# Optimization experiments

Measured on AMD Instinct MI355X. Metric: run time of the kernel, lower is better.

Reference implementation:

```python
import jax, jax.numpy as jnp
import numpy as np
from math import sqrt

# Complete K-ary tree: level l has K**l nodes; children of node j at level l
# are nodes j*K .. j*K+K-1 of level l+1. Levels are processed leaves->root.
K = 4
LEVELS = 9
N_NODES = (K ** LEVELS - 1) // (K - 1)  # 87381
X_SIZE = 256
H_SIZE = 256
A_SIZE = 256
N_HEADS = 8
A_K = A_SIZE // N_HEADS


def setup_inputs() -> dict:
    key = jax.random.key(0)
    ks = jax.random.split(key, 20)
    s = 0.02
    d = {
        'x': jax.random.normal(ks[0], (N_NODES, X_SIZE), dtype=jnp.float32),
        'W_iou': jax.random.normal(ks[1], (X_SIZE, 3 * H_SIZE), dtype=jnp.float32) * s,
        'b_iou': jnp.zeros((3 * H_SIZE,), dtype=jnp.float32),
        'W_f': jax.random.normal(ks[2], (X_SIZE, H_SIZE), dtype=jnp.float32) * s,
        'b_f': jnp.zeros((H_SIZE,), dtype=jnp.float32),
        'Wq': jax.random.normal(ks[3], (X_SIZE, A_SIZE), dtype=jnp.float32) * s,
        'bq': jax.random.normal(ks[4], (A_SIZE,), dtype=jnp.float32) * s,
        'Wk': jax.random.normal(ks[5], (H_SIZE, A_SIZE), dtype=jnp.float32) * s,
        'bk': jax.random.normal(ks[6], (A_SIZE,), dtype=jnp.float32) * s,
        'Wv': jax.random.normal(ks[7], (H_SIZE, A_SIZE), dtype=jnp.float32) * s,
        'bv': jax.random.normal(ks[8], (A_SIZE,), dtype=jnp.float32) * s,
        'Wl': jax.random.normal(ks[9], (A_SIZE, A_SIZE), dtype=jnp.float32) * s,
        'bl': jax.random.normal(ks[10], (A_SIZE,), dtype=jnp.float32) * s,
        'Uiou_w': jax.random.normal(ks[11], (A_SIZE, 3 * H_SIZE), dtype=jnp.float32) * s,
        'Uiou_b': jax.random.normal(ks[12], (3 * H_SIZE,), dtype=jnp.float32) * s,
        'Uf_w': jax.random.normal(ks[13], (A_SIZE, H_SIZE), dtype=jnp.float32) * s,
        'Uf_b': jax.random.normal(ks[14], (H_SIZE,), dtype=jnp.float32) * s,
    }
    return d


def _tree_lstm(x, W_iou, b_iou, W_f, b_f, Wq, bq, Wk, bk, Wv, bv, Wl, bl,
               Uiou_w, Uiou_b, Uf_w, Uf_b):
    scale = 1.0 / sqrt(A_K)
    x_iou = x @ W_iou + b_iou          # [N, 3H]
    x_f = x @ W_f + b_f                # [N, H]
    starts = [(K ** l - 1) // (K - 1) for l in range(LEVELS)]
    h_lvl = [None] * LEVELS
    c_lvl = [None] * LEVELS
    for l in reversed(range(LEVELS)):
        s0 = starts[l]
        n = K ** l
        xi = x_iou[s0:s0 + n]
        xf = x_f[s0:s0 + n]
        if l == LEVELS - 1:  # leaves: empty mailbox
            iou = xi
            fc_sum = jnp.zeros((n, H_SIZE), dtype=x.dtype)
        else:
            ch_h = h_lvl[l + 1].reshape(n, K, H_SIZE)  # children mailbox 'h'
            ch_c = c_lvl[l + 1].reshape(n, K, H_SIZE)  # children mailbox 'c'
            q = (x[s0:s0 + n] @ Wq + bq).reshape(n, N_HEADS, A_K)
            kk = (ch_h @ Wk + bk).reshape(n, K, N_HEADS, A_K)
            vv = (ch_h @ Wv + bv).reshape(n, K, N_HEADS, A_K)
            logits = jnp.einsum('nhd,nkhd->nhk', q, kk) * scale
            attn = jax.nn.softmax(logits, axis=-1)
            out = jnp.einsum('nhk,nkhd->nhd', attn, vv).reshape(n, A_SIZE)
            h_attn = out @ Wl + bl
            h_iou = h_attn @ Uiou_w + Uiou_b
            h_f = h_attn @ Uf_w + Uf_b
            f = jax.nn.sigmoid(xf + h_f)[:, None, :]   # same f for all children
            fc_sum = jnp.sum(ch_c * f, axis=1)
            iou = xi + h_iou
        i, o, u = jnp.split(iou, 3, axis=1)
        c_new = jax.nn.sigmoid(i) * jnp.tanh(u) + fc_sum
        h_new = jax.nn.sigmoid(o) * jnp.tanh(c_new)
        h_lvl[l] = h_new
        c_lvl[l] = c_new
    h = jnp.concatenate(h_lvl, axis=0)
    c = jnp.concatenate(c_lvl, axis=0)
    return h, c


def reference(x, W_iou, b_iou, W_f, b_f, Wq, bq, Wk, bk, Wv, bv, Wl, bl,
              Uiou_w, Uiou_b, Uf_w, Uf_b):
    return _tree_lstm(x, W_iou, b_iou, W_f, b_f, Wq, bq, Wk, bk, Wv, bv,
                      Wl, bl, Uiou_w, Uiou_b, Uf_w, Uf_b)
```

## Files before the change

kernel.cpp:

```cpp
#include <hip/hip_runtime.h>
#include <hip/hip_bf16.h>
#include <math.h>

constexpr int LEVELS_ = 9;
constexpr int N_NODES_ = 87381;
constexpr int HS = 256;
constexpr int N_HEADS_ = 8;

typedef __attribute__((ext_vector_type(8))) short bf16x8;
typedef __attribute__((ext_vector_type(4))) float f32x4;
typedef __attribute__((ext_vector_type(4))) float float4v;

__device__ __forceinline__ short f2bf(float f) {
    union { float f; unsigned u; } a; a.f = f;
    unsigned r = (a.u + 0x7fff + ((a.u >> 16) & 1)) >> 16;
    return (short)r;
}
__device__ __forceinline__ float bf2f(short s) {
    union { unsigned u; float f; } a; a.u = ((unsigned)(unsigned short)s) << 16;
    return a.f;
}
__device__ __forceinline__ float sigm(float x) { return 1.f / (1.f + __expf(-x)); }
__device__ __forceinline__ float ftanh(float x) {
    float e = __expf(-2.f * fabsf(x));
    float t = (1.f - e) / (1.f + e);
    return copysignf(t, x);
}

__device__ __forceinline__ void gl_lds16(const short* g, short* l) {
    __builtin_amdgcn_global_load_lds(
        (const __attribute__((address_space(1))) void*)g,
        (__attribute__((address_space(3))) void*)l, 16, 0, 0);
}

__device__ __forceinline__ int xcd_swizzle(int flat, int nwg) {
    int q = nwg >> 3, r = nwg & 7;
    int xcd = flat & 7, idx = flat >> 3;
    int base = (xcd < r) ? xcd * (q + 1) : r * (q + 1) + (xcd - r) * q;
    return base + idx;
}

__device__ __forceinline__ void gridbar(int* c, int nb) {
    __syncthreads();
    if (threadIdx.x == 0) {
        __threadfence();
        atomicAdd(c, 1);
        while (atomicAdd(c, 0) < nb) __builtin_amdgcn_s_sleep(2);
        __threadfence();
    }
    __syncthreads();
}

__global__ __launch_bounds__(256) void gemm_bf16(
    const short* __restrict__ A, const short* __restrict__ Bt,
    const float* __restrict__ bias, const short* __restrict__ Cadd,
    void* __restrict__ Cout, int M, int N, int Kd, int out_bf16,
    short* __restrict__ Cout2, int Nsplit)
{
    __shared__ __align__(16) short smem[32768];

    const int tid = threadIdx.x;
    const int lane = tid & 63;
    const int w = tid >> 6;
    const int gx = gridDim.x;
    const int sw = xcd_swizzle(blockIdx.y * gx + blockIdx.x, gx * gridDim.y);
    const int row0 = (sw / gx) * 128;
    const int col0 = (sw % gx) * 128;
    const int wm = (w >> 1) * 64;
    const int wn = (w & 1) * 64;
    const int q = lane >> 4;
    const int mr = lane & 15;

    const int srl = lane >> 3;
    const int scs = ((lane & 7) ^ srl) * 8;

    auto stage = [&](int b, int k0) {
        short* As = smem + b * 16384;
        short* Bs = As + 8192;
        #pragma unroll
        for (int i = 0; i < 4; ++i) {
            int s = w * 4 + i;
            int r = s * 8 + srl;
            gl_lds16(A + (size_t)(row0 + r) * Kd + k0 + scs, As + s * 512);
            gl_lds16(Bt + (size_t)(col0 + r) * Kd + k0 + scs, Bs + s * 512);
        }
    };

    f32x4 acc[4][4];
    #pragma unroll
    for (int i = 0; i < 4; i++)
        #pragma unroll
        for (int j = 0; j < 4; j++) acc[i][j] = (f32x4){0.f, 0.f, 0.f, 0.f};

    stage(0, 0);
    __syncthreads();
    const int nk = Kd >> 6;
    for (int t = 0; t < nk; ++t) {
        if (t + 1 < nk) stage((t + 1) & 1, (t + 1) << 6);
        const short* As = smem + (t & 1) * 16384;
        const short* Bs = As + 8192;
        #pragma unroll
        for (int h = 0; h < 2; ++h) {
            bf16x8 af[4], bfr[4];
            #pragma unroll
            for (int i = 0; i < 4; ++i) {
                int r = wm + i * 16 + mr;
                af[i] = *(const bf16x8*)(As + r * 64 + ((h * 4 + q) ^ (mr & 7)) * 8);
            }
            #pragma unroll
            for (int j = 0; j < 4; ++j) {
                int r = wn + j * 16 + mr;
                bfr[j] = *(const bf16x8*)(Bs + r * 64 + ((h * 4 + q) ^ (mr & 7)) * 8);
            }
            #pragma unroll
            for (int i = 0; i < 4; ++i)
                #pragma unroll
                for (int j = 0; j < 4; ++j)
                    acc[i][j] = __builtin_amdgcn_mfma_f32_16x16x32_bf16(
                        af[i], bfr[j], acc[i][j], 0, 0, 0);
        }
        __syncthreads();
    }

    short* dst;
    int width, colbase;
    if (Cout2 && col0 >= Nsplit) { dst = Cout2; colbase = col0 - Nsplit; width = N - Nsplit; }
    else { dst = (short*)Cout; colbase = col0; width = Cout2 ? Nsplit : N; }

    if (out_bf16) {
        short* Cs = smem;
        #pragma unroll
        for (int j = 0; j < 4; ++j) {
            int col = wn + j * 16 + mr;
            float bv = bias ? bias[col0 + col] : 0.f;
            #pragma unroll
            for (int i = 0; i < 4; ++i) {
                #pragma unroll
                for (int r = 0; r < 4; ++r) {
                    int lr = wm + i * 16 + q * 4 + r;
                    float v = acc[i][j][r] + bv;
                    if (Cadd && row0 + lr < M)
                        v += bf2f(Cadd[(size_t)(row0 + lr) * width + colbase + col]);
                    Cs[lr * 128 + col] = f2bf(v);
                }
            }
        }
        __syncthreads();
        #pragma unroll
        for (int i = 0; i < 8; ++i) {
            int chunk = i * 256 + tid;
            int lr = chunk >> 4;
            int c8 = (chunk & 15) * 8;
            if (row0 + lr < M)
                *(bf16x8*)(dst + (size_t)(row0 + lr) * width + colbase + c8) =
                    *(const bf16x8*)(Cs + lr * 128 + c8);
        }
    } else {
        #pragma unroll
        for (int j = 0; j < 4; ++j) {
            int col = col0 + wn + j * 16 + mr;
            float bv = bias ? bias[col] : 0.f;
            #pragma unroll
            for (int i = 0; i < 4; ++i) {
                #pragma unroll
                for (int r = 0; r < 4; ++r) {
                    int grow = row0 + wm + i * 16 + q * 4 + r;
                    if (grow < M) {
                        size_t off = (size_t)grow * N + col;
                        float v = acc[i][j][r] + bv;
                        if (Cadd) v += bf2f(Cadd[off]);
                        ((float*)Cout)[off] = v;
                    }
                }
            }
        }
    }
}

__global__ __launch_bounds__(256) void gemm_cell(
    const short* __restrict__ A, const short* __restrict__ Bt,
    const float* __restrict__ bias, const short* __restrict__ Cadd,
    const float* __restrict__ c_child,
    float* __restrict__ h_out, float* __restrict__ c_out,
    short* __restrict__ hb_out, int M)
{
    __shared__ __align__(16) short smem[32768];

    const int tid = threadIdx.x;
    const int lane = tid & 63;
    const int w = tid >> 6;
    const int gx = gridDim.x;
    const int sw = xcd_swizzle(blockIdx.y * gx + blockIdx.x, gx * gridDim.y);
    const int row0 = (sw / gx) * 128;
    const int bxs = sw % gx;
    const int col0 = bxs * 128;
    const int wm = (w >> 1) * 64;
    const int wn = (w & 1) * 64;
    const int q = lane >> 4;
    const int mr = lane & 15;

    const int srl = lane >> 3;
    const int scs = ((lane & 7) ^ srl) * 8;

    const bool leaf = (c_child == nullptr);
    const int jn = (leaf && wn == 64) ? 2 : 4;

    auto stage = [&](int b, int k0) {
        short* As = smem + b * 16384;
        short* Bs = As + 8192;
        #pragma unroll
        for (int i = 0; i < 4; ++i) {
            int s = w * 4 + i;
            int r = s * 8 + srl;
            gl_lds16(A + (size_t)(row0 + r) * 256 + k0 + scs, As + s * 512);
            if (!(leaf && s >= 12))
                gl_lds16(Bt + (size_t)(col0 + r) * 256 + k0 + scs, Bs + s * 512);
        }
    };

    f32x4 acc[4][4];
    #pragma unroll
    for (int i = 0; i < 4; i++)
        #pragma unroll
        for (int j = 0; j < 4; j++) acc[i][j] = (f32x4){0.f, 0.f, 0.f, 0.f};

    stage(0, 0);
    __syncthreads();
    for (int t = 0; t < 4; ++t) {
        if (t + 1 < 4) stage((t + 1) & 1, (t + 1) << 6);
        const short* As = smem + (t & 1) * 16384;
        const short* Bs = As + 8192;
        #pragma unroll
        for (int h = 0; h < 2; ++h) {
            bf16x8 af[4], bfr[4];
            #pragma unroll
            for (int i = 0; i < 4; ++i) {
                int r = wm + i * 16 + mr;
                af[i] = *(const bf16x8*)(As + r * 64 + ((h * 4 + q) ^ (mr & 7)) * 8);
            }
            #pragma unroll
            for (int j = 0; j < 4; ++j)
                if (j < jn) {
                    int r = wn + j * 16 + mr;
                    bfr[j] = *(const bf16x8*)(Bs + r * 64 + ((h * 4 + q) ^ (mr & 7)) * 8);
                }
            #pragma unroll
            for (int i = 0; i < 4; ++i)
                #pragma unroll
                for (int j = 0; j < 4; ++j)
                    if (j < jn)
                        acc[i][j] = __builtin_amdgcn_mfma_f32_16x16x32_bf16(
                            af[i], bfr[j], acc[i][j], 0, 0, 0);
        }
        __syncthreads();
    }

    short* Cs = smem;
    #pragma unroll
    for (int j = 0; j < 4; ++j) {
        int col = wn + j * 16 + mr;
        float bv = bias[col0 + col];
        #pragma unroll
        for (int i = 0; i < 4; ++i) {
            #pragma unroll
            for (int r = 0; r < 4; ++r) {
                int lr = wm + i * 16 + q * 4 + r;
                float v = acc[i][j][r] + bv;
                if (Cadd && row0 + lr < M)
                    v += bf2f(Cadd[(size_t)(row0 + lr) * 1024 + col0 + col]);
                Cs[lr * 136 + col] = f2bf(v);
            }
        }
    }
    __syncthreads();

    const int hd0 = bxs * 32;
    #pragma unroll 1
    for (int it = 0; it < 2; ++it) {
        int chunk = it * 256 + tid;
        int row = chunk >> 2;
        int d8 = (chunk & 3) * 8;
        int gp = row0 + row;
        if (gp < M) {
            bf16x8 vi = *(const bf16x8*)(Cs + row * 136 + d8);
            bf16x8 vo = *(const bf16x8*)(Cs + row * 136 + 32 + d8);
            bf16x8 vu = *(const bf16x8*)(Cs + row * 136 + 64 + d8);
            float fc[8] = {0.f, 0.f, 0.f, 0.f, 0.f, 0.f, 0.f, 0.f};
            if (!leaf) {
                bf16x8 vf = *(const bf16x8*)(Cs + row * 136 + 96 + d8);
                #pragma unroll
                for (int c = 0; c < 4; ++c) {
                    const float* cp = c_child + (size_t)(4 * gp + c) * 256 + hd0 + d8;
                    float4v a = *(const float4v*)cp;
                    float4v b = *(const float4v*)(cp + 4);
                    #pragma unroll
                    for (int e = 0; e < 4; ++e) { fc[e] += a[e]; fc[4 + e] += b[e]; }
                }
                #pragma unroll
                for (int e = 0; e < 8; ++e) fc[e] *= sigm(bf2f(vf[e]));
            }
            float4v hv[2], cv[2];
            bf16x8 hbv;
            #pragma unroll
            for (int e = 0; e < 8; ++e) {
                float cn = sigm(bf2f(vi[e])) * ftanh(bf2f(vu[e])) + fc[e];
                float hn = sigm(bf2f(vo[e])) * ftanh(cn);
                hv[e >> 2][e & 3] = hn;
                cv[e >> 2][e & 3] = cn;
                hbv[e] = f2bf(hn);
            }
            size_t o = (size_t)gp * 256 + hd0 + d8;
            *(float4v*)(h_out + o) = hv[0]; *(float4v*)(h_out + o + 4) = hv[1];
            *(float4v*)(c_out + o) = cv[0]; *(float4v*)(c_out + o + 4) = cv[1];
            *(bf16x8*)(hb_out + o) = hbv;
        }
    }
}

__global__ __launch_bounds__(256) void kv_attn(
    const short* __restrict__ A,
    const short* __restrict__ B3t,
    const float* __restrict__ bias_kv,
    const short* __restrict__ qb_lvl,
    short* __restrict__ outb)
{
    __shared__ __align__(16) short smem[32768 + 2048];
    short* sh_o = smem + 32768;

    const int tid = threadIdx.x;
    const int lane = tid & 63;
    const int w = tid >> 6;
    const int gx = gridDim.x;
    const int sw = xcd_swizzle(blockIdx.y * gx + blockIdx.x, gx * gridDim.y);
    const int byq = sw / gx;
    const int colb = sw % gx;
    const int row0 = byq * 128;
    const int col0 = colb * 128;
    const int wm = (w >> 1) * 64;
    const int wn = (w & 1) * 64;
    const int q = lane >> 4;
    const int mr = lane & 15;

    const int srl = lane >> 3;
    const int scs = ((lane & 7) ^ srl) * 8;

    auto stage = [&](int b, int k0) {
        short* As = smem + b * 16384;
        short* Bs = As + 8192;
        #pragma unroll
        for (int i = 0; i < 4; ++i) {
            int s = w * 4 + i;
            int r = s * 8 + srl;
            gl_lds16(A + (size_t)(row0 + r) * 256 + k0 + scs, As + s * 512);
            gl_lds16(B3t + (size_t)(col0 + r) * 256 + k0 + scs, Bs + s * 512);
        }
    };

    f32x4 acc[4][4];
    #pragma unroll
    for (int i = 0; i < 4; i++)
        #pragma unroll
        for (int j = 0; j < 4; j++) acc[i][j] = (f32x4){0.f, 0.f, 0.f, 0.f};

    stage(0, 0);
    __syncthreads();
    for (int t = 0; t < 4; ++t) {
        if (t + 1 < 4) stage((t + 1) & 1, (t + 1) << 6);
        const short* As = smem + (t & 1) * 16384;
        const short* Bs = As + 8192;
        #pragma unroll
        for (int h = 0; h < 2; ++h) {
            bf16x8 af[4], bfr[4];
            #pragma unroll
            for (int i = 0; i < 4; ++i) {
                int r = wm + i * 16 + mr;
                af[i] = *(const bf16x8*)(As + r * 64 + ((h * 4 + q) ^ (mr & 7)) * 8);
            }
            #pragma unroll
            for (int j = 0; j < 4; ++j) {
                int r = wn + j * 16 + mr;
                bfr[j] = *(const bf16x8*)(Bs + r * 64 + ((h * 4 + q) ^ (mr & 7)) * 8);
            }
            #pragma unroll
            for (int i = 0; i < 4; ++i)
                #pragma unroll
                for (int j = 0; j < 4; ++j)
                    acc[i][j] = __builtin_amdgcn_mfma_f32_16x16x32_bf16(
                        af[i], bfr[j], acc[i][j], 0, 0, 0);
        }
        __syncthreads();
    }

    short* Cs = smem;
    #pragma unroll
    for (int j = 0; j < 4; ++j) {
        int col = wn + j * 16 + mr;
        float bv = bias_kv[col0 + col];
        #pragma unroll
        for (int i = 0; i < 4; ++i) {
            #pragma unroll
            for (int r = 0; r < 4; ++r) {
                int lr = wm + i * 16 + q * 4 + r;
                Cs[lr * 128 + col] = f2bf(acc[i][j][r] + bv);
            }
        }
    }
    __syncthreads();

    const int p0 = byq * 32;
    const int grp0 = tid >> 5;
    const int l32 = tid & 31;
    #pragma unroll 1
    for (int it = 0; it < 8; ++it) {
        int pair = it * 8 + grp0;
        int pl = pair >> 1, hh = pair & 1;
        float qv = bf2f(qb_lvl[(size_t)(p0 + pl) * 256 + (colb * 2 + hh) * 32 + l32]);
        float logit[4];
        #pragma unroll
        for (int c = 0; c < 4; ++c) {
            float pch = qv * bf2f(Cs[(4 * pl + c) * 128 + hh * 64 + l32]);
            #pragma unroll
            for (int off = 16; off >= 1; off >>= 1)
                pch += __shfl_xor(pch, off, 32);
            logit[c] = pch * 0.17677669529663687f;
        }
        float mx = fmaxf(fmaxf(logit[0], logit[1]), fmaxf(logit[2], logit[3]));
        float e[4], s = 0.f;
        #pragma unroll
        for (int c = 0; c < 4; ++c) { e[c] = __expf(logit[c] - mx); s += e[c]; }
        float inv = 1.f / s;
        float o = 0.f;
        #pragma unroll
        for (int c = 0; c < 4; ++c)
            o += (e[c] * inv) * bf2f(Cs[(4 * pl + c) * 128 + hh * 64 + 32 + l32]);
        sh_o[pl * 64 + hh * 32 + l32] = f2bf(o);
    }
    __syncthreads();
    {
        int r = tid >> 3, c8 = (tid & 7) * 8;
        *(bf16x8*)(outb + (size_t)(p0 + r) * 256 + colb * 64 + c8) =
            *(const bf16x8*)(sh_o + r * 64 + c8);
    }
}

__global__ __launch_bounds__(256) void level_fused_all(
    short* hb, float* c_all,
    const short* __restrict__ qb, const short* __restrict__ xi,
    const short* __restrict__ B3t, const short* __restrict__ Wlt,
    const short* __restrict__ Bt2,
    const float* __restrict__ bias_kv, const float* __restrict__ bl,
    const float* __restrict__ biasU,
    float* h_all, int* bar)
{
    __shared__ __align__(16) char smem[50176];
    short* sh_h    = (short*)smem;
    short* sh_kv   = (short*)(smem + 16896);
    short* sh_out  = (short*)smem;
    short* sh_ha   = (short*)(smem + 8448);
    float* sh_iouf = (float*)(smem + 16896);

    const int tid = threadIdx.x;
    const int lane = tid & 63;
    const int w = tid >> 6;
    const int q = lane >> 4;
    const int mr = lane & 15;

    static constexpr int st[7] = {0, 1, 5, 21, 85, 341, 1365};

    for (int l = 5; l >= 0; --l) {
        const int n  = 1 << (2 * l);
        const int s0 = st[l];
        const int sc = st[l + 1];
        const int p0 = blockIdx.x * 8;
        if (p0 < n) {
            const int np = (n - p0 < 8) ? (n - p0) : 8;
            const int nch = 4 * np;

            #pragma unroll
            for (int i = 0; i < 4; ++i) {
                int chunk = i * 256 + tid;
                int r = chunk >> 5;
                int c8 = (chunk & 31) * 8;
                bf16x8 v = {};
                if (r < nch) v = *(const bf16x8*)(hb + (size_t)(sc + 4 * p0 + r) * 256 + c8);
                *(bf16x8*)(sh_h + r * 264 + c8) = v;
            }
            __syncthreads();

            {
                f32x4 acc[2][8];
                #pragma unroll
                for (int rt = 0; rt < 2; ++rt)
                    #pragma unroll
                    for (int ct = 0; ct < 8; ++ct) acc[rt][ct] = (f32x4){0.f, 0.f, 0.f, 0.f};
                #pragma unroll 1
                for (int k0 = 0; k0 < 256; k0 += 32) {
                    bf16x8 a0 = *(const bf16x8*)(sh_h + mr * 264 + k0 + q * 8);
                    bf16x8 a1 = *(const bf16x8*)(sh_h + (16 + mr) * 264 + k0 + q * 8);
                    #pragma unroll
                    for (int ct = 0; ct < 8; ++ct) {
                        int col = w * 128 + ct * 16 + mr;
                        bf16x8 b = *(const bf16x8*)(B3t + (size_t)col * 256 + k0 + q * 8);
                        acc[0][ct] = __builtin_amdgcn_mfma_f32_16x16x32_bf16(a0, b, acc[0][ct], 0, 0, 0);
                        acc[1][ct] = __builtin_amdgcn_mfma_f32_16x16x32_bf16(a1, b, acc[1][ct], 0, 0, 0);
                    }
                }
                #pragma unroll
                for (int ct = 0; ct < 8; ++ct) {
                    int col = w * 128 + ct * 16 + mr;
                    float bv = bias_kv[col];
                    #pragma unroll
                    for (int rt = 0; rt < 2; ++rt)
                        #pragma unroll
                        for (int r = 0; r < 4; ++r) {
                            int row = rt * 16 + q * 4 + r;
                            sh_kv[row * 520 + col] = f2bf(acc[rt][ct][r] + bv);
                        }
                }
            }
            __syncthreads();

            {
                const int grp0 = tid >> 5;
                const int l32 = tid & 31;
                #pragma unroll 1
                for (int it = 0; it < 8; ++it) {
                    int grp = it * 8 + grp0;
                    int node = grp >> 3, head = grp & 7;
                    if (node < np) {
                        float qv = bf2f(qb[(size_t)(s0 + p0 + node) * 256 + head * 32 + l32]);
                        float logit[4];
                        #pragma unroll
                        for (int c = 0; c < 4; ++c) {
                            float p = qv * bf2f(sh_kv[(4 * node + c) * 520 + head * 64 + l32]);
                            #pragma unroll
                            for (int off = 16; off >= 1; off >>= 1)
                                p += __shfl_xor(p, off, 32);
                            logit[c] = p * 0.17677669529663687f;
                        }
                        float mx = fmaxf(fmaxf(logit[0], logit[1]), fmaxf(logit[2], logit[3]));
                        float e[4], s = 0.f;
                        #pragma unroll
                        for (int c = 0; c < 4; ++c) { e[c] = __expf(logit[c] - mx); s += e[c]; }
                        float inv = 1.f / s;
                        float o = 0.f;
                        #pragma unroll
                        for (int c = 0; c < 4; ++c)
                            o += (e[c] * inv) * bf2f(sh_kv[(4 * node + c) * 520 + head * 64 + 32 + l32]);
                        sh_out[node * 264 + head * 32 + l32] = f2bf(o);
                    }
                }
            }
            __syncthreads();

            {
                f32x4 acc[4];
                #pragma unroll
                for (int ct = 0; ct < 4; ++ct) acc[ct] = (f32x4){0.f, 0.f, 0.f, 0.f};
                #pragma unroll 1
                for (int k0 = 0; k0 < 256; k0 += 32) {
                    bf16x8 a = *(const bf16x8*)(sh_out + mr * 264 + k0 + q * 8);
                    #pragma unroll
                    for (int ct = 0; ct < 4; ++ct) {
                        int col = w * 64 + ct * 16 + mr;
                        bf16x8 b = *(const bf16x8*)(Wlt + (size_t)col * 256 + k0 + q * 8);
                        acc[ct] = __builtin_amdgcn_mfma_f32_16x16x32_bf16(a, b, acc[ct], 0, 0, 0);
                    }
                }
                #pragma unroll
                for (int ct = 0; ct < 4; ++ct) {
                    int col = w * 64 + ct * 16 + mr;
                    float bv = bl[col];
                    #pragma unroll
                    for (int r = 0; r < 4; ++r) {
                        int row = q * 4 + r;
                        if (row < np) sh_ha[row * 264 + col] = f2bf(acc[ct][r] + bv);
                    }
                }
            }
            __syncthreads();

            {
                f32x4 acc[16];
                #pragma unroll
                for (int ct = 0; ct < 16; ++ct) acc[ct] = (f32x4){0.f, 0.f, 0.f, 0.f};
                #pragma unroll 1
                for (int k0 = 0; k0 < 256; k0 += 32) {
                    bf16x8 a = *(const bf16x8*)(sh_ha + mr * 264 + k0 + q * 8);
                    #pragma unroll
                    for (int ct = 0; ct < 16; ++ct) {
                        int col = w * 256 + ct * 16 + mr;
                        bf16x8 b = *(const bf16x8*)(Bt2 + (size_t)col * 256 + k0 + q * 8);
                        acc[ct] = __builtin_amdgcn_mfma_f32_16x16x32_bf16(a, b, acc[ct], 0, 0, 0);
                    }
                }
                __syncthreads();
                #pragma unroll
                for (int ct = 0; ct < 16; ++ct) {
                    int col = w * 256 + ct * 16 + mr;
                    float bU = biasU[col];
                    #pragma unroll
                    for (int r = 0; r < 4; ++r) {
                        int row = q * 4 + r;
                        if (row < np)
                            sh_iouf[row * 1024 + col] =
                                acc[ct][r] + bU + bf2f(xi[(size_t)(s0 + p0 + row) * 1024 + col]);
                    }
                }
            }
            __syncthreads();

            #pragma unroll 1
            for (int it = 0; it < 8; ++it) {
                int t = it * 256 + tid;
                if (t < np * 256) {
                    int node = t >> 8, j = t & 255;
                    int gcol = (j >> 5) * 128 + (j & 31);
                    float iv = sh_iouf[node * 1024 + gcol];
                    float ov = sh_iouf[node * 1024 + gcol + 32];
                    float uv = sh_iouf[node * 1024 + gcol + 64];
                    float fv = sigm(sh_iouf[node * 1024 + gcol + 96]);
                    float fc = 0.f;
                    #pragma unroll
                    for (int c = 0; c < 4; ++c)
                        fc += c_all[(size_t)(sc + 4 * (p0 + node) + c) * 256 + j] * fv;
                    float cn = sigm(iv) * ftanh(uv) + fc;
                    float hn = sigm(ov) * ftanh(cn);
                    size_t o = (size_t)(s0 + p0 + node) * 256 + j;
                    h_all[o] = hn;
                    c_all[o] = cn;
                    hb[o] = f2bf(hn);
                }
            }
        }
        if (l > 0) gridbar(bar + (5 - l), gridDim.x);
    }
}

__global__ __launch_bounds__(256) void conv_x(
    const float* __restrict__ x, short* __restrict__ xb, int n8)
{
    int t = blockIdx.x * 256 + threadIdx.x;
    if (t >= n8) return;
    float4v a = *(const float4v*)(x + (size_t)t * 8);
    float4v b = *(const float4v*)(x + (size_t)t * 8 + 4);
    bf16x8 o;
    o[0] = f2bf(a.x); o[1] = f2bf(a.y); o[2] = f2bf(a.z); o[3] = f2bf(a.w);
    o[4] = f2bf(b.x); o[5] = f2bf(b.y); o[6] = f2bf(b.z); o[7] = f2bf(b.w);
    *(bf16x8*)(xb + (size_t)t * 8) = o;
}

__global__ __launch_bounds__(256) void prep_weights(
    const float* __restrict__ W_iou, const float* __restrict__ W_f,
    const float* __restrict__ Uiou_w, const float* __restrict__ Uf_w,
    const float* __restrict__ Wk, const float* __restrict__ Wv,
    const float* __restrict__ Wq, const float* __restrict__ Wl,
    const float* __restrict__ b_iou, const float* __restrict__ b_f,
    const float* __restrict__ Uiou_b, const float* __restrict__ Uf_b,
    const float* __restrict__ bk, const float* __restrict__ bv,
    const float* __restrict__ bq,
    short* __restrict__ Bt1, short* __restrict__ Bt2, short* __restrict__ B3t,
    short* __restrict__ Wqt, short* __restrict__ Wlt,
    float* __restrict__ biasX, float* __restrict__ biasU,
    float* __restrict__ bias_kv, int* __restrict__ bar)
{
    int t = blockIdx.x * 256 + threadIdx.x;
    if (t < 262144) {
        int gc = t >> 8, k = t & 255;
        int within = gc & 127, gate = within >> 5, d = (gc >> 7) * 32 + (within & 31);
        float v = (gate < 3) ? W_iou[k * 768 + gate * 256 + d] : W_f[k * 256 + d];
        Bt1[t] = f2bf(v);
        return;
    }
    t -= 262144;
    if (t < 262144) {
        int gc = t >> 8, k = t & 255;
        int within = gc & 127, gate = within >> 5, d = (gc >> 7) * 32 + (within & 31);
        float v = (gate < 3) ? Uiou_w[k * 768 + gate * 256 + d] : Uf_w[k * 256 + d];
        Bt2[t] = f2bf(v);
        return;
    }
    t -= 262144;
    if (t < 131072) {
        int gc = t >> 8, k = t & 255;
        int head = gc >> 6, kv = (gc >> 5) & 1, d = head * 32 + (gc & 31);
        float v = kv ? Wv[k * 256 + d] : Wk[k * 256 + d];
        B3t[t] = f2bf(v);
        return;
    }
    t -= 131072;
    if (t < 65536) { int nn = t >> 8, k = t & 255; Wqt[t] = f2bf(Wq[k * 256 + nn]); return; }
    t -= 65536;
    if (t < 65536) { int nn = t >> 8, k = t & 255; Wlt[t] = f2bf(Wl[k * 256 + nn]); return; }
    t -= 65536;
    if (t < 1024) {
        int within = t & 127, gate = within >> 5, d = (t >> 7) * 32 + (within & 31);
        biasX[t] = (gate < 3) ? b_iou[gate * 256 + d] : b_f[d];
        return;
    }
    t -= 1024;
    if (t < 256) { biasX[1024 + t] = bq[t]; return; }
    t -= 256;
    if (t < 1024) {
        int within = t & 127, gate = within >> 5, d = (t >> 7) * 32 + (within & 31);
        biasU[t] = (gate < 3) ? Uiou_b[gate * 256 + d] : Uf_b[d];
        return;
    }
    t -= 1024;
    if (t < 512) {
        int head = t >> 6, kv = (t >> 5) & 1, d = head * 32 + (t & 31);
        bias_kv[t] = kv ? bv[d] : bk[d];
        return;
    }
    t -= 512;
    if (t < 8) { bar[t] = 0; return; }
}

static inline void launch_gemm(const short* A, const short* Bt, const float* bias,
                               const short* Cadd, void* C, int M, int N, int Kd,
                               int out_bf16, short* C2, int Nsplit, hipStream_t stream)
{
    dim3 grid(N / 128, (M + 127) / 128);
    gemm_bf16<<<grid, 256, 0, stream>>>(A, Bt, bias, Cadd, C, M, N, Kd, out_bf16,
                                        C2, Nsplit);
}

extern "C" void kernel_launch(void* const* d_in, const int* in_sizes, int n_in,
                              void* d_out, int out_size, void* d_ws, size_t ws_size,
                              hipStream_t stream)
{
    const float* x      = (const float*)d_in[0];
    const float* W_iou  = (const float*)d_in[1];
    const float* b_iou  = (const float*)d_in[2];
    const float* W_f    = (const float*)d_in[3];
    const float* b_f    = (const float*)d_in[4];
    const float* Wq     = (const float*)d_in[5];
    const float* bq     = (const float*)d_in[6];
    const float* Wk     = (const float*)d_in[7];
    const float* bk     = (const float*)d_in[8];
    const float* Wv     = (const float*)d_in[9];
    const float* bv     = (const float*)d_in[10];
    const float* Wl     = (const float*)d_in[11];
    const float* bl     = (const float*)d_in[12];
    const float* Uiou_w = (const float*)d_in[13];
    const float* Uiou_b = (const float*)d_in[14];
    const float* Uf_w   = (const float*)d_in[15];
    const float* Uf_b   = (const float*)d_in[16];

    float* h_all = (float*)d_out;
    float* c_all = h_all + (size_t)N_NODES_ * HS;

    char* p = (char*)d_ws;
    short* xb   = (short*)p; p += (size_t)N_NODES_ * 256 * 2;
    short* hb   = (short*)p; p += (size_t)N_NODES_ * 256 * 2;
    short* xi   = (short*)p; p += (size_t)21845 * 1024 * 2;
    short* qb   = (short*)p; p += (size_t)21845 * 256 * 2;
    short* outb = (short*)p; p += (size_t)16384 * 256 * 2;
    short* hab  = (short*)p; p += (size_t)16384 * 256 * 2;
    short* Bt1  = (short*)p; p += (size_t)1024 * 256 * 2;
    short* Wqt  = (short*)p; p += (size_t)256 * 256 * 2;
    short* Bt2  = (short*)p; p += (size_t)1024 * 256 * 2;
    short* B3t  = (short*)p; p += (size_t)512 * 256 * 2;
    short* Wlt  = (short*)p; p += (size_t)256 * 256 * 2;
    float* biasX   = (float*)p; p += 1280 * 4;
    float* biasU   = (float*)p; p += 1024 * 4;
    float* bias_kv = (float*)p; p += 512 * 4;
    int*   bar     = (int*)p;   p += 8 * 4;

    static const int starts[LEVELS_] = {0, 1, 5, 21, 85, 341, 1365, 5461, 21845};

    {
        int n8 = N_NODES_ * 256 / 8;
        conv_x<<<(n8 + 255) / 256, 256, 0, stream>>>(x, xb, n8);
        int total = 262144 + 262144 + 131072 + 65536 + 65536 + 1024 + 256 + 1024 + 512 + 8;
        prep_weights<<<(total + 255) / 256, 256, 0, stream>>>(
            W_iou, W_f, Uiou_w, Uf_w, Wk, Wv, Wq, Wl,
            b_iou, b_f, Uiou_b, Uf_b, bk, bv, bq,
            Bt1, Bt2, B3t, Wqt, Wlt, biasX, biasU, bias_kv, bar);
    }

    launch_gemm(xb, Bt1, biasX, nullptr, xi, 21845, 1280, 256, 1, qb, 1024, stream);

    {
        dim3 grid(8, 65536 / 128);
        gemm_cell<<<grid, 256, 0, stream>>>(
            xb + (size_t)21845 * 256, Bt1, biasX, nullptr, nullptr,
            h_all + (size_t)21845 * HS, c_all + (size_t)21845 * HS,
            hb + (size_t)21845 * HS, 65536);
    }

    for (int l = 7; l >= 6; l--) {
        int n  = 1 << (2 * l);
        int s0 = starts[l];
        int sc = starts[l + 1];
        int nc = 4 * n;

        dim3 gkv(4, nc / 128);
        kv_attn<<<gkv, 256, 0, stream>>>(
            hb + (size_t)sc * 256, B3t, bias_kv, qb + (size_t)s0 * 256, outb);
        launch_gemm(outb, Wlt, bl, nullptr, hab, n, 256, 256, 1, nullptr, 0, stream);
        dim3 gc(8, n / 128);
        gemm_cell<<<gc, 256, 0, stream>>>(
            hab, Bt2, biasU, xi + (size_t)s0 * 1024, c_all + (size_t)sc * HS,
            h_all + (size_t)s0 * HS, c_all + (size_t)s0 * HS,
            hb + (size_t)s0 * HS, n);
    }

    level_fused_all<<<128, 256, 0, stream>>>(
        hb, c_all, qb, xi, B3t, Wlt, Bt2, bias_kv, bl, biasU, h_all, bar);
}
```

Baseline: 877.5 us.

## Replace persistent grid-barrier kernel with per-level launches for upper tree levels

Drops the single persistent kernel that handled levels 5..0 with software grid barriers built on atomics. Instead it launches one fused kernel per level, with exactly ceil(n/8) blocks, so kernel boundaries provide the ordering. This removes the spin-wait barriers and idle blocks on small levels, at the cost of six kernel launch overheads. Barrier counter initialisation is removed from weight prep.

Result: faster. 843.0 us (-3.9%).

```diff
diff --git a/kernel.cpp b/kernel.cpp
--- a/kernel.cpp
+++ b/kernel.cpp
@@ -38,17 +38,6 @@
     int xcd = flat & 7, idx = flat >> 3;
     int base = (xcd < r) ? xcd * (q + 1) : r * (q + 1) + (xcd - r) * q;
     return base + idx;
-}
-
-__device__ __forceinline__ void gridbar(int* c, int nb) {
-    __syncthreads();
-    if (threadIdx.x == 0) {
-        __threadfence();
-        atomicAdd(c, 1);
-        while (atomicAdd(c, 0) < nb) __builtin_amdgcn_s_sleep(2);
-        __threadfence();
-    }
-    __syncthreads();
 }
 
 __global__ __launch_bounds__(256) void gemm_bf16(
@@ -443,14 +432,15 @@
     }
 }
 
-__global__ __launch_bounds__(256) void level_fused_all(
-    short* hb, float* c_all,
+__global__ __launch_bounds__(256) void level_fused(
+    const short* __restrict__ hb, const float* __restrict__ c_all,
     const short* __restrict__ qb, const short* __restrict__ xi,
     const short* __restrict__ B3t, const short* __restrict__ Wlt,
     const short* __restrict__ Bt2,
     const float* __restrict__ bias_kv, const float* __restrict__ bl,
     const float* __restrict__ biasU,
-    float* h_all, int* bar)
+    float* __restrict__ h_all, float* __restrict__ c_out_g,
+    short* __restrict__ hb_out, int s0, int sc, int n)
 {
     __shared__ __align__(16) char smem[50176];
     short* sh_h    = (short*)smem;
@@ -464,176 +454,165 @@
     const int w = tid >> 6;
     const int q = lane >> 4;
     const int mr = lane & 15;
-
-    static constexpr int st[7] = {0, 1, 5, 21, 85, 341, 1365};
-
-    for (int l = 5; l >= 0; --l) {
-        const int n  = 1 << (2 * l);
-        const int s0 = st[l];
-        const int sc = st[l + 1];
-        const int p0 = blockIdx.x * 8;
-        if (p0 < n) {
-            const int np = (n - p0 < 8) ? (n - p0) : 8;
-            const int nch = 4 * np;
-
-            #pragma unroll
-            for (int i = 0; i < 4; ++i) {
-                int chunk = i * 256 + tid;
-                int r = chunk >> 5;
-                int c8 = (chunk & 31) * 8;
-                bf16x8 v = {};
-                if (r < nch) v = *(const bf16x8*)(hb + (size_t)(sc + 4 * p0 + r) * 256 + c8);
-                *(bf16x8*)(sh_h + r * 264 + c8) = v;
-            }
-            __syncthreads();
-
-            {
-                f32x4 acc[2][8];
-                #pragma unroll
-                for (int rt = 0; rt < 2; ++rt)
+    const int p0 = blockIdx.x * 8;
+    const int np = (n - p0 < 8) ? (n - p0) : 8;
+    const int nch = 4 * np;
+
+    #pragma unroll
+    for (int i = 0; i < 4; ++i) {
+        int chunk = i * 256 + tid;
+        int r = chunk >> 5;
+        int c8 = (chunk & 31) * 8;
+        bf16x8 v = {};
+        if (r < nch) v = *(const bf16x8*)(hb + (size_t)(sc + 4 * p0 + r) * 256 + c8);
+        *(bf16x8*)(sh_h + r * 264 + c8) = v;
+    }
+    __syncthreads();
+
+    {
+        f32x4 acc[2][8];
+        #pragma unroll
+        for (int rt = 0; rt < 2; ++rt)
+            #pragma unroll
+            for (int ct = 0; ct < 8; ++ct) acc[rt][ct] = (f32x4){0.f, 0.f, 0.f, 0.f};
+        #pragma unroll 1
+        for (int k0 = 0; k0 < 256; k0 += 32) {
+            bf16x8 a0 = *(const bf16x8*)(sh_h + mr * 264 + k0 + q * 8);
+            bf16x8 a1 = *(const bf16x8*)(sh_h + (16 + mr) * 264 + k0 + q * 8);
+            #pragma unroll
+            for (int ct = 0; ct < 8; ++ct) {
+                int col = w * 128 + ct * 16 + mr;
+                bf16x8 b = *(const bf16x8*)(B3t + (size_t)col * 256 + k0 + q * 8);
+                acc[0][ct] = __builtin_amdgcn_mfma_f32_16x16x32_bf16(a0, b, acc[0][ct], 0, 0, 0);
+                acc[1][ct] = __builtin_amdgcn_mfma_f32_16x16x32_bf16(a1, b, acc[1][ct], 0, 0, 0);
+            }
+        }
+        #pragma unroll
+        for (int ct = 0; ct < 8; ++ct) {
+            int col = w * 128 + ct * 16 + mr;
+            float bv = bias_kv[col];
+            #pragma unroll
+            for (int rt = 0; rt < 2; ++rt)
+                #pragma unroll
+                for (int r = 0; r < 4; ++r) {
+                    int row = rt * 16 + q * 4 + r;
+                    sh_kv[row * 520 + col] = f2bf(acc[rt][ct][r] + bv);
+                }
+        }
+    }
+    __syncthreads();
+
+    {
+        const int grp0 = tid >> 5;
+        const int l32 = tid & 31;
+        #pragma unroll 1
+        for (int it = 0; it < 8; ++it) {
+            int grp = it * 8 + grp0;
+            int node = grp >> 3, head = grp & 7;
+            if (node < np) {
+                float qv = bf2f(qb[(size_t)(s0 + p0 + node) * 256 + head * 32 + l32]);
+                float logit[4];
+                #pragma unroll
+                for (int c = 0; c < 4; ++c) {
+                    float p = qv * bf2f(sh_kv[(4 * node + c) * 520 + head * 64 + l32]);
                     #pragma unroll
-                    for (int ct = 0; ct < 8; ++ct) acc[rt][ct] = (f32x4){0.f, 0.f, 0.f, 0.f};
-                #pragma unroll 1
-                for (int k0 = 0; k0 < 256; k0 += 32) {
-                    bf16x8 a0 = *(const bf16x8*)(sh_h + mr * 264 + k0 + q * 8);
-                    bf16x8 a1 = *(const bf16x8*)(sh_h + (16 + mr) * 264 + k0 + q * 8);
-                    #pragma unroll
-                    for (int ct = 0; ct < 8; ++ct) {
-                        int col = w * 128 + ct * 16 + mr;
-                        bf16x8 b = *(const bf16x8*)(B3t + (size_t)col * 256 + k0 + q * 8);
-                        acc[0][ct] = __builtin_amdgcn_mfma_f32_16x16x32_bf16(a0, b, acc[0][ct], 0, 0, 0);
-                        acc[1][ct] = __builtin_amdgcn_mfma_f32_16x16x32_bf16(a1, b, acc[1][ct], 0, 0, 0);
-                    }
+                    for (int off = 16; off >= 1; off >>= 1)
+                        p += __shfl_xor(p, off, 32);
+                    logit[c] = p * 0.17677669529663687f;
                 }
-                #pragma unroll
-                for (int ct = 0; ct < 8; ++ct) {
-                    int col = w * 128 + ct * 16 + mr;
-                    float bv = bias_kv[col];
-                    #pragma unroll
-                    for (int rt = 0; rt < 2; ++rt)
-                        #pragma unroll
-                        for (int r = 0; r < 4; ++r) {
-                            int row = rt * 16 + q * 4 + r;
-                            sh_kv[row * 520 + col] = f2bf(acc[rt][ct][r] + bv);
-                        }
-                }
-            }
-            __syncthreads();
-
-            {
-                const int grp0 = tid >> 5;
-                const int l32 = tid & 31;
-                #pragma unroll 1
-                for (int it = 0; it < 8; ++it) {
-                    int grp = it * 8 + grp0;
-                    int node = grp >> 3, head = grp & 7;
-                    if (node < np) {
-                        float qv = bf2f(qb[(size_t)(s0 + p0 + node) * 256 + head * 32 + l32]);
-                        float logit[4];
-                        #pragma unroll
-                        for (int c = 0; c < 4; ++c) {
-                            float p = qv * bf2f(sh_kv[(4 * node + c) * 520 + head * 64 + l32]);
-                            #pragma unroll
-                            for (int off = 16; off >= 1; off >>= 1)
-                                p += __shfl_xor(p, off, 32);
-                            logit[c] = p * 0.17677669529663687f;
-                        }
-                        float mx = fmaxf(fmaxf(logit[0], logit[1]), fmaxf(logit[2], logit[3]));
-                        float e[4], s = 0.f;
-                        #pragma unroll
-                        for (int c = 0; c < 4; ++c) { e[c] = __expf(logit[c] - mx); s += e[c]; }
-                        float inv = 1.f / s;
-                        float o = 0.f;
-                        #pragma unroll
-                        for (int c = 0; c < 4; ++c)
-                            o += (e[c] * inv) * bf2f(sh_kv[(4 * node + c) * 520 + head * 64 + 32 + l32]);
-                        sh_out[node * 264 + head * 32 + l32] = f2bf(o);
-                    }
-                }
-            }
-            __syncthreads();
-
-            {
-                f32x4 acc[4];
-                #pragma unroll
-                for (int ct = 0; ct < 4; ++ct) acc[ct] = (f32x4){0.f, 0.f, 0.f, 0.f};
-                #pragma unroll 1
-                for (int k0 = 0; k0 < 256; k0 += 32) {
-                    bf16x8 a = *(const bf16x8*)(sh_out + mr * 264 + k0 + q * 8);
-                    #pragma unroll
-                    for (int ct = 0; ct < 4; ++ct) {
-                        int col = w * 64 + ct * 16 + mr;
-                        bf16x8 b = *(const bf16x8*)(Wlt + (size_t)col * 256 + k0 + q * 8);
-                        acc[ct] = __builtin_amdgcn_mfma_f32_16x16x32_bf16(a, b, acc[ct], 0, 0, 0);
-                    }
-                }
-                #pragma unroll
-                for (int ct = 0; ct < 4; ++ct) {
-                    int col = w * 64 + ct * 16 + mr;
-                    float bv = bl[col];
-                    #pragma unroll
-                    for (int r = 0; r < 4; ++r) {
-                        int row = q * 4 + r;
-                        if (row < np) sh_ha[row * 264 + col] = f2bf(acc[ct][r] + bv);
-                    }
-                }
-            }
-            __syncthreads();
-
-            {
-                f32x4 acc[16];
-                #pragma unroll
-                for (int ct = 0; ct < 16; ++ct) acc[ct] = (f32x4){0.f, 0.f, 0.f, 0.f};
-                #pragma unroll 1
-                for (int k0 = 0; k0 < 256; k0 += 32) {
-                    bf16x8 a = *(const bf16x8*)(sh_ha + mr * 264 + k0 + q * 8);
-                    #pragma unroll
-                    for (int ct = 0; ct < 16; ++ct) {
-                        int col = w * 256 + ct * 16 + mr;
-                        bf16x8 b = *(const bf16x8*)(Bt2 + (size_t)col * 256 + k0 + q * 8);
-                        acc[ct] = __builtin_amdgcn_mfma_f32_16x16x32_bf16(a, b, acc[ct], 0, 0, 0);
-                    }
-                }
-                __syncthreads();
-                #pragma unroll
-                for (int ct = 0; ct < 16; ++ct) {
-                    int col = w * 256 + ct * 16 + mr;
-                    float bU = biasU[col];
-                    #pragma unroll
-                    for (int r = 0; r < 4; ++r) {
-                        int row = q * 4 + r;
-                        if (row < np)
-                            sh_iouf[row * 1024 + col] =
-                                acc[ct][r] + bU + bf2f(xi[(size_t)(s0 + p0 + row) * 1024 + col]);
-                    }
-                }
-            }
-            __syncthreads();
-
-            #pragma unroll 1
-            for (int it = 0; it < 8; ++it) {
-                int t = it * 256 + tid;
-                if (t < np * 256) {
-                    int node = t >> 8, j = t & 255;
-                    int gcol = (j >> 5) * 128 + (j & 31);
-                    float iv = sh_iouf[node * 1024 + gcol];
-                    float ov = sh_iouf[node * 1024 + gcol + 32];
-                    float uv = sh_iouf[node * 1024 + gcol + 64];
-                    float fv = sigm(sh_iouf[node * 1024 + gcol + 96]);
-                    float fc = 0.f;
-                    #pragma unroll
-                    for (int c = 0; c < 4; ++c)
-                        fc += c_all[(size_t)(sc + 4 * (p0 + node) + c) * 256 + j] * fv;
-                    float cn = sigm(iv) * ftanh(uv) + fc;
-                    float hn = sigm(ov) * ftanh(cn);
-                    size_t o = (size_t)(s0 + p0 + node) * 256 + j;
-                    h_all[o] = hn;
-                    c_all[o] = cn;
-                    hb[o] = f2bf(hn);
-                }
-            }
-        }
-        if (l > 0) gridbar(bar + (5 - l), gridDim.x);
+                float mx = fmaxf(fmaxf(logit[0], logit[1]), fmaxf(logit[2], logit[3]));
+                float e[4], s = 0.f;
+                #pragma unroll
+                for (int c = 0; c < 4; ++c) { e[c] = __expf(logit[c] - mx); s += e[c]; }
+                float inv = 1.f / s;
+                float o = 0.f;
+                #pragma unroll
+                for (int c = 0; c < 4; ++c)
+                    o += (e[c] * inv) * bf2f(sh_kv[(4 * node + c) * 520 + head * 64 + 32 + l32]);
+                sh_out[node * 264 + head * 32 + l32] = f2bf(o);
+            }
+        }
+    }
+    __syncthreads();
+
+    {
+        f32x4 acc[4];
+        #pragma unroll
+        for (int ct = 0; ct < 4; ++ct) acc[ct] = (f32x4){0.f, 0.f, 0.f, 0.f};
+        #pragma unroll 1
+        for (int k0 = 0; k0 < 256; k0 += 32) {
+            bf16x8 a = *(const bf16x8*)(sh_out + mr * 264 + k0 + q * 8);
+            #pragma unroll
+            for (int ct = 0; ct < 4; ++ct) {
+                int col = w * 64 + ct * 16 + mr;
+                bf16x8 b = *(const bf16x8*)(Wlt + (size_t)col * 256 + k0 + q * 8);
+                acc[ct] = __builtin_amdgcn_mfma_f32_16x16x32_bf16(a, b, acc[ct], 0, 0, 0);
+            }
+        }
+        #pragma unroll
+        for (int ct = 0; ct < 4; ++ct) {
+            int col = w * 64 + ct * 16 + mr;
+            float bv = bl[col];
+            #pragma unroll
+            for (int r = 0; r < 4; ++r) {
+                int row = q * 4 + r;
+                if (row < np) sh_ha[row * 264 + col] = f2bf(acc[ct][r] + bv);
+            }
+        }
+    }
+    __syncthreads();
+
+    {
+        f32x4 acc[16];
+        #pragma unroll
+        for (int ct = 0; ct < 16; ++ct) acc[ct] = (f32x4){0.f, 0.f, 0.f, 0.f};
+        #pragma unroll 1
+        for (int k0 = 0; k0 < 256; k0 += 32) {
+            bf16x8 a = *(const bf16x8*)(sh_ha + mr * 264 + k0 + q * 8);
+            #pragma unroll
+            for (int ct = 0; ct < 16; ++ct) {
+                int col = w * 256 + ct * 16 + mr;
+                bf16x8 b = *(const bf16x8*)(Bt2 + (size_t)col * 256 + k0 + q * 8);
+                acc[ct] = __builtin_amdgcn_mfma_f32_16x16x32_bf16(a, b, acc[ct], 0, 0, 0);
+            }
+        }
+        __syncthreads();
+        #pragma unroll
+        for (int ct = 0; ct < 16; ++ct) {
+            int col = w * 256 + ct * 16 + mr;
+            float bU = biasU[col];
+            #pragma unroll
+            for (int r = 0; r < 4; ++r) {
+                int row = q * 4 + r;
+                if (row < np)
+                    sh_iouf[row * 1024 + col] =
+                        acc[ct][r] + bU + bf2f(xi[(size_t)(s0 + p0 + row) * 1024 + col]);
+            }
+        }
+    }
+    __syncthreads();
+
+    #pragma unroll 1
+    for (int it = 0; it < 8; ++it) {
+        int t = it * 256 + tid;
+        if (t < np * 256) {
+            int node = t >> 8, j = t & 255;
+            int gcol = (j >> 5) * 128 + (j & 31);
+            float iv = sh_iouf[node * 1024 + gcol];
+            float ov = sh_iouf[node * 1024 + gcol + 32];
+            float uv = sh_iouf[node * 1024 + gcol + 64];
+            float fv = sigm(sh_iouf[node * 1024 + gcol + 96]);
+            float fc = 0.f;
+            #pragma unroll
+            for (int c = 0; c < 4; ++c)
+                fc += c_all[(size_t)(sc + 4 * (p0 + node) + c) * 256 + j] * fv;
+            float cn = sigm(iv) * ftanh(uv) + fc;
+            float hn = sigm(ov) * ftanh(cn);
+            size_t o = (size_t)(s0 + p0 + node) * 256 + j;
+            h_all[o] = hn;
+            c_out_g[o] = cn;
+            hb_out[o] = f2bf(hn);
+        }
     }
 }
 
@@ -662,7 +641,7 @@
     short* __restrict__ Bt1, short* __restrict__ Bt2, short* __restrict__ B3t,
     short* __restrict__ Wqt, short* __restrict__ Wlt,
     float* __restrict__ biasX, float* __restrict__ biasU,
-    float* __restrict__ bias_kv, int* __restrict__ bar)
+    float* __restrict__ bias_kv)
 {
     int t = blockIdx.x * 256 + threadIdx.x;
     if (t < 262144) {
@@ -712,8 +691,6 @@
         bias_kv[t] = kv ? bv[d] : bk[d];
         return;
     }
-    t -= 512;
-    if (t < 8) { bar[t] = 0; return; }
 }
 
 static inline void launch_gemm(const short* A, const short* Bt, const float* bias,
@@ -765,18 +742,17 @@
     float* biasX   = (float*)p; p += 1280 * 4;
     float* biasU   = (float*)p; p += 1024 * 4;
     float* bias_kv = (float*)p; p += 512 * 4;
-    int*   bar     = (int*)p;   p += 8 * 4;
 
     static const int starts[LEVELS_] = {0, 1, 5, 21, 85, 341, 1365, 5461, 21845};
 
     {
         int n8 = N_NODES_ * 256 / 8;
         conv_x<<<(n8 + 255) / 256, 256, 0, stream>>>(x, xb, n8);
-        int total = 262144 + 262144 + 131072 + 65536 + 65536 + 1024 + 256 + 1024 + 512 + 8;
+        int total = 262144 + 262144 + 131072 + 65536 + 65536 + 1024 + 256 + 1024 + 512;
         prep_weights<<<(total + 255) / 256, 256, 0, stream>>>(
             W_iou, W_f, Uiou_w, Uf_w, Wk, Wv, Wq, Wl,
             b_iou, b_f, Uiou_b, Uf_b, bk, bv, bq,
-            Bt1, Bt2, B3t, Wqt, Wlt, biasX, biasU, bias_kv, bar);
+            Bt1, Bt2, B3t, Wqt, Wlt, biasX, biasU, bias_kv);
     }
 
     launch_gemm(xb, Bt1, biasX, nullptr, xi, 21845, 1280, 256, 1, qb, 1024, stream);
@@ -806,6 +782,13 @@
             hb + (size_t)s0 * HS, n);
     }
 
-    level_fused_all<<<128, 256, 0, stream>>>(
-        hb, c_all, qb, xi, B3t, Wlt, Bt2, bias_kv, bl, biasU, h_all, bar);
-}
+    for (int l = 5; l >= 0; l--) {
+        int n  = 1 << (2 * l);
+        int s0 = starts[l];
+        int sc = starts[l + 1];
+        int blocks = (n + 7) / 8;
+        level_fused<<<blocks, 256, 0, stream>>>(
+            hb, c_all, qb, xi, B3t, Wlt, Bt2, bias_kv, bl, biasU,
+            h_all, c_all, hb, s0, sc, n);
+    }
+}
```
